# Kernel tuning notes

Hardware: AMD Instinct MI355X
Metric: run time of the kernel (lower is better)

The kernel has to match this reference:

```python
import jax, jax.numpy as jnp
import numpy as np

BIG = 1e9  # finite stand-in for float('inf') border padding (grad-safe)


def setup_inputs() -> dict:
    key = jax.random.key(0)
    k1, k2 = jax.random.split(key)
    B, L1, L2, F = 32, 1024, 1024, 128
    return {
        "seq1": jax.random.normal(k1, (B, L1, F), dtype=jnp.float32),
        "seq2": jax.random.normal(k2, (B, L2, F), dtype=jnp.float32),
        "scale_weights": jnp.ones((1,), dtype=jnp.float32),  # nn.Parameter ones(num_scales)/num_scales -> softmax-normalized anyway
    }


def _dtw_similarity(seq1, seq2):
    """Vectorized (anti-diagonal wavefront) version of MultiScaleDTW._compute_dtw.

    Same recurrence: D[i,j] = ||s1[i-1]-s2[j-1]|| + min(D[i-1,j-1], D[i-1,j], D[i,j-1]),
    D[0,0]=0, first row/col = inf. Returns similarity = 1/(1 + D[L1,L2]/(L1+L2)).
    """
    B, L1, F = seq1.shape
    L2 = seq2.shape[1]
    # pairwise L2 distance matrix (B, L1, L2) via |a|^2 + |b|^2 - 2 a.b (one GEMM)
    sq1 = jnp.sum(seq1 * seq1, axis=-1)
    sq2 = jnp.sum(seq2 * seq2, axis=-1)
    dot = jnp.einsum('bif,bjf->bij', seq1, seq2)
    C = jnp.sqrt(jnp.maximum(sq1[:, :, None] + sq2[:, None, :] - 2.0 * dot, 0.0))

    i_idx = jnp.arange(L1 + 1)
    # diagonal k holds D[i, k-i] for i in [0, L1]
    d0 = jnp.full((B, L1 + 1), BIG, jnp.float32).at[:, 0].set(0.0)  # k=0: D[0,0]=0
    d1 = jnp.full((B, L1 + 1), BIG, jnp.float32)                     # k=1: borders = inf

    def shift(x):  # x[:, i] -> x[:, i-1], pad with BIG
        return jnp.concatenate([jnp.full((B, 1), BIG, x.dtype), x[:, :-1]], axis=1)

    def step(carry, k):
        prev2, prev = carry  # diagonals k-2, k-1
        j = k - i_idx
        row = jnp.clip(i_idx - 1, 0, L1 - 1)
        col = jnp.clip(j - 1, 0, L2 - 1)
        c = C[:, row, col]  # (B, L1+1) cost along the diagonal
        m = jnp.minimum(shift(prev2), jnp.minimum(shift(prev), prev))
        cur = c + m
        valid = (i_idx >= 1) & (i_idx <= L1) & (j >= 1) & (j <= L2)
        cur = jnp.where(valid[None, :], cur, BIG)
        return (prev, cur), None

    (_, last), _ = jax.lax.scan(step, (d0, d1), jnp.arange(2, L1 + L2 + 1))
    dtw_dist = last[:, L1] / (L1 + L2)  # D[L1, L2] / (L1 + L2)
    return 1.0 / (1.0 + dtw_dist)


def reference(seq1, seq2, scale_weights):
    # num_scales = 1: softmax over single scale weight -> 1.0; only scale-0 DTW runs
    w = jax.nn.softmax(scale_weights, axis=0)
    sim = _dtw_similarity(seq1, seq2)
    return w[0] * sim  # combined_similarity, shape (B,)
```

## Files before the change

kernel.cpp:

```cpp
#include <hip/hip_runtime.h>
#include <hip/hip_bf16.h>

#define BIGV 1.0e9f

static constexpr int B_ = 32;
static constexpr int L_ = 1024;
static constexpr int F_ = 128;
static constexpr int S_ = 2;
static constexpr int UDIM_ = 1296;
static constexpr int LAG_ = 256;
static constexpr int NSEGG_ = 22;
static constexpr size_t STREAM_US = (size_t)B_ * 2 * UDIM_ * 512;

typedef __attribute__((ext_vector_type(8))) short short8;
typedef __attribute__((ext_vector_type(4))) float f32x4;

__device__ __forceinline__ unsigned pack2(float x, float y) {
  unsigned r;
  asm("v_cvt_pk_bf16_f32 %0, %1, %2" : "=v"(r) : "v"(x), "v"(y));
  return r;
}

__device__ __forceinline__ float shfl_up1_dpp(float x) {
  int xi = __float_as_int(x);
  int r = __builtin_amdgcn_update_dpp(xi, xi, 0x138, 0xF, 0xF, false);
  return __int_as_float(r);
}

__device__ __forceinline__ float min3f(float a, float b, float c) {
  float r;
  asm("v_min3_f32 %0, %1, %2, %3" : "=v"(r) : "v"(a), "v"(b), "v"(c));
  return r;
}

__global__ void norm_kernel(const float* __restrict__ s1, const float* __restrict__ s2,
                            float* __restrict__ nrm) {
  int gt   = blockIdx.x * blockDim.x + threadIdx.x;
  int wid  = gt >> 6;
  int lane = gt & 63;
  const float* src = (wid < B_ * L_) ? (s1 + (size_t)wid * F_)
                                     : (s2 + (size_t)(wid - B_ * L_) * F_);
  float2 v = ((const float2*)src)[lane];
  float s = v.x * v.x + v.y * v.y;
#pragma unroll
  for (int o = 32; o > 0; o >>= 1) s += __shfl_xor(s, o, 64);
  if (lane == 0) nrm[wid] = s;
}

__global__ __launch_bounds__(256) void cost_kernel(const float* __restrict__ s1,
                                                   const float* __restrict__ s2,
                                                   ushort* __restrict__ stream,
                                                   const float* __restrict__ nrm) {
  __shared__ __align__(16) ushort sbuf[2 * 128 * 136];
  __shared__ float q1[128], q2[128];
  short (*aL)[136] = (short(*)[136])sbuf;
  short (*bL)[136] = (short(*)[136])(sbuf + 128 * 136);
  ushort (*stage)[136] = (ushort(*)[136])sbuf;

  const int tid = threadIdx.x;
  const int b   = blockIdx.y;
  const int tc  = blockIdx.x & 7;
  const int tr  = blockIdx.x >> 3;

  const float* Ap = s1 + (size_t)b * L_ * F_ + (size_t)tr * 128 * F_;
  const float* Bp = s2 + (size_t)b * L_ * F_ + (size_t)tc * 128 * F_;

#pragma unroll 4
  for (int it = 0; it < 16; ++it) {
    int idx = it * 1024 + tid * 4;
    int r = idx >> 7, cc = idx & 127;
    float4 va = *(const float4*)(Ap + idx);
    float4 vb = *(const float4*)(Bp + idx);
    *(uint2*)&aL[r][cc] = make_uint2(pack2(va.x, va.y), pack2(va.z, va.w));
    *(uint2*)&bL[r][cc] = make_uint2(pack2(vb.x, vb.y), pack2(vb.z, vb.w));
  }
  if (tid < 128) q1[tid] = nrm[(size_t)b * L_ + tr * 128 + tid];
  else           q2[tid - 128] = nrm[(size_t)B_ * L_ + (size_t)b * L_ + tc * 128 + (tid - 128)];
  __syncthreads();

  const int wave = tid >> 6, lane = tid & 63, quad = lane >> 4, l16 = lane & 15;
  const int m0 = (wave >> 1) * 64, n0 = (wave & 1) * 64;

  f32x4 acc[4][4] = {};
#pragma unroll
  for (int kc = 0; kc < 4; ++kc) {
    short8 af[4], bf[4];
#pragma unroll
    for (int mi = 0; mi < 4; ++mi)
      af[mi] = *(const short8*)&aL[m0 + mi * 16 + l16][kc * 32 + quad * 8];
#pragma unroll
    for (int nj = 0; nj < 4; ++nj)
      bf[nj] = *(const short8*)&bL[n0 + nj * 16 + l16][kc * 32 + quad * 8];
#pragma unroll
    for (int mi = 0; mi < 4; ++mi)
#pragma unroll
      for (int nj = 0; nj < 4; ++nj)
        acc[mi][nj] = __builtin_amdgcn_mfma_f32_16x16x32_bf16(af[mi], bf[nj], acc[mi][nj], 0, 0, 0);
  }

  __syncthreads();

#pragma unroll
  for (int mi = 0; mi < 4; ++mi) {
    int lr = m0 + mi * 16 + quad * 4;
    int du = 2 * (lr >> 3);
    float a0 = q1[lr + 0], a1 = q1[lr + 1], a2 = q1[lr + 2], a3 = q1[lr + 3];
#pragma unroll
    for (int nj = 0; nj < 4; ++nj) {
      int lc = n0 + nj * 16 + l16;
      float qc = q2[lc];
      float vx = sqrtf(fmaxf(a0 + qc - 2.0f * acc[mi][nj][0], 0.0f));
      float vy = sqrtf(fmaxf(a1 + qc - 2.0f * acc[mi][nj][1], 0.0f));
      float vz = sqrtf(fmaxf(a2 + qc - 2.0f * acc[mi][nj][2], 0.0f));
      float vw = sqrtf(fmaxf(a3 + qc - 2.0f * acc[mi][nj][3], 0.0f));
      *(uint2*)&stage[lc + du][lr] = make_uint2(pack2(vx, vy), pack2(vz, vw));
    }
  }
  __syncthreads();

  const int w      = tr >> 2;
  const int rlbase = (tr & 3) * 128;
  const int ubase  = tc * 128 + 32 * (tr & 3);
  ushort* Sb = stream + ((size_t)(b * 2 + w) * UDIM_ + ubase) * 512 + rlbase;
#pragma unroll
  for (int it = 0; it < 10; ++it) {
    int t = it * 256 + tid;
    if (t < 158 * 16) {
      int u = t >> 4, g = t & 15;
      if ((unsigned)(u - 2 * g) < 128u)
        *(uint4*)(Sb + (size_t)u * 512 + g * 8) = *(const uint4*)&stage[u][g * 8];
    }
  }
}

#define UNPACK_CV(cw, cv)                         \
  cv[0] = __uint_as_float((cw).x << 16);          \
  cv[1] = __uint_as_float((cw).x & 0xFFFF0000u);  \
  cv[2] = __uint_as_float((cw).y << 16);          \
  cv[3] = __uint_as_float((cw).y & 0xFFFF0000u);  \
  cv[4] = __uint_as_float((cw).z << 16);          \
  cv[5] = __uint_as_float((cw).z & 0xFFFF0000u);  \
  cv[6] = __uint_as_float((cw).w << 16);          \
  cv[7] = __uint_as_float((cw).w & 0xFFFF0000u);

#define CHAIN_BODY(head)                                            \
  {                                                                 \
    float cur = (head);                                             \
    float nl[8];                                                    \
    nl[0] = cur;                                                    \
    _Pragma("unroll") for (int r = 1; r < 8; ++r) {                 \
      cur = cv[r] + min3f(left[r - 1], left[r], cur);               \
      nl[r] = cur;                                                  \
    }                                                               \
    _Pragma("unroll") for (int r = 0; r < 8; ++r) left[r] = nl[r];  \
    bot = nl[7];                                                    \
  }

__global__ __launch_bounds__(128, 1) void dtw_kernel(const ushort* __restrict__ stream,
                                                     float* __restrict__ out) {
  __shared__ float hand[1040];

  const int b    = blockIdx.x;
  const int tid  = threadIdx.x;
  const int wave = tid >> 6;
  const int lane = tid & 63;
  const bool l0 = (lane == 0);

  const ushort* src = stream + (size_t)(b * 2 + wave) * UDIM_ * 512 + lane * 8;

  float left[8];
#pragma unroll
  for (int r = 0; r < 8; ++r) left[r] = BIGV;
  float bot = BIGV;
  float sh[4] = {BIGV, BIGV, BIGV, BIGV};
  float hPrev = BIGV, result = 0.0f;
  float hRing[4];
  float hb[16];
  uint4 pre[16];

#pragma unroll
  for (int i = 0; i < 16; ++i) pre[i] = *(const uint4*)(src + (size_t)i * 512);

  for (int n = 0; n < NSEGG_; ++n) {
    __syncthreads();
    const int phaseS = 64 * n - (wave ? LAG_ : 0);

#pragma unroll 1
    for (int m = 0; m < 4; ++m) {
      const int sBase = phaseS + 16 * m;
      if ((unsigned)sBase >= 1152u) continue;

      const bool fast = (sBase >= 128) & (sBase <= 1008);

      if (wave == 0) {
        if (fast) {
#pragma unroll
          for (int k = 0; k < 16; ++k) {
            float shN = shfl_up1_dpp(bot);
            uint4 cw = pre[k];
            pre[k] = *(const uint4*)(src + (size_t)(sBase + k + 16) * 512);
            float cv[8];
            UNPACK_CV(cw, cv)
            float dgT = sh[(k + 2) & 3];
            float upT = sh[(k + 3) & 3];
            CHAIN_BODY(cv[0] + min3f(dgT, upT, left[0]))
            sh[k & 3] = l0 ? BIGV : shN;
            hb[k] = bot;
          }
          if (lane == 63) {
            float4* hp = (float4*)&hand[sBase - 126];
            hp[0] = make_float4(hb[0], hb[1], hb[2], hb[3]);
            hp[1] = make_float4(hb[4], hb[5], hb[6], hb[7]);
            hp[2] = make_float4(hb[8], hb[9], hb[10], hb[11]);
            hp[3] = make_float4(hb[12], hb[13], hb[14], hb[15]);
          }
        } else {
#pragma unroll
          for (int k = 0; k < 16; ++k) {
            const int s = sBase + k;
            const int col = s - S_ * lane;
            float shN = shfl_up1_dpp(bot);
            uint4 cw = pre[k];
            pre[k] = *(const uint4*)(src + (size_t)(sBase + k + 16) * 512);
            float cv[8];
            UNPACK_CV(cw, cv)
            float dgT = sh[(k + 2) & 3];
            if (l0 && s == 0) dgT = 0.0f;
            float upT = sh[(k + 3) & 3];
            bool act = ((unsigned)col < 1024u);
            float c0 = act ? cv[0] : BIGV;
            CHAIN_BODY(c0 + min3f(dgT, upT, left[0]))
            sh[k & 3] = l0 ? BIGV : shN;
            int j = s - 126;
            if (lane == 63 && (unsigned)j < 1024u) hand[j] = bot;
          }
        }
      } else {
        if (fast) {
#pragma unroll
          for (int i = 0; i < 4; ++i) hRing[i] = hand[sBase + i];
#pragma unroll
          for (int k = 0; k < 16; ++k) {
            float shN = shfl_up1_dpp(bot);
            float hCur = hRing[k & 3];
            uint4 cw = pre[k];
            pre[k] = *(const uint4*)(src + (size_t)(sBase + k + 16) * 512);
            hRing[k & 3] = hand[sBase + k + 4];
            float cv[8];
            UNPACK_CV(cw, cv)
            float dgT = l0 ? hPrev : sh[(k + 2) & 3];
            float upT = l0 ? hCur : sh[(k + 3) & 3];
            CHAIN_BODY(cv[0] + min3f(dgT, upT, left[0]))
            sh[k & 3] = shN;
            hPrev = hCur;
          }
        } else {
#pragma unroll
          for (int i = 0; i < 4; ++i) hRing[i] = hand[(sBase + i) & 1023];
#pragma unroll
          for (int k = 0; k < 16; ++k) {
            const int s = sBase + k;
            const int col = s - S_ * lane;
            float shN = shfl_up1_dpp(bot);
            float hCur = hRing[k & 3];
            uint4 cw = pre[k];
            pre[k] = *(const uint4*)(src + (size_t)(sBase + k + 16) * 512);
            hRing[k & 3] = hand[(s + 4) & 1023];
            float cv[8];
            UNPACK_CV(cw, cv)
            float dgT = l0 ? ((s == 0) ? BIGV : hPrev) : sh[(k + 2) & 3];
            float upT = l0 ? hCur : sh[(k + 3) & 3];
            bool act = ((unsigned)col < 1024u);
            float c0 = act ? cv[0] : BIGV;
            CHAIN_BODY(c0 + min3f(dgT, upT, left[0]))
            sh[k & 3] = shN;
            hPrev = hCur;
            if (s == 1149) result = bot;
          }
        }
      }
    }
  }
  if (wave == 1 && lane == 63) out[b] = 1.0f / (1.0f + result * (1.0f / 2048.0f));
}

extern "C" void kernel_launch(void* const* d_in, const int* in_sizes, int n_in,
                              void* d_out, int out_size, void* d_ws, size_t ws_size,
                              hipStream_t stream_) {
  const float* s1 = (const float*)d_in[0];
  const float* s2 = (const float*)d_in[1];
  float* out = (float*)d_out;
  ushort* cws = (ushort*)d_ws;
  float* nrm = (float*)(cws + STREAM_US);

  norm_kernel<<<dim3((2 * B_ * L_) / 4), 256, 0, stream_>>>(s1, s2, nrm);
  cost_kernel<<<dim3(64, B_), 256, 0, stream_>>>(s1, s2, cws, nrm);
  dtw_kernel<<<dim3(B_), 128, 0, stream_>>>(cws, out);
}
```

Before: 236.8 us.

## Process two DTW columns per lane per step with paired cost stream layout

Each lane now handles two adjacent columns per wavefront step instead of one. This halves the number of serial steps, from a skew of 2 per lane to 1 per lane, and shortens the inter-wave lag. The cost kernel pairs adjacent columns with a DPP swap and writes interleaved bf16 pairs into a re-laid-out stream. The aim is to cut the wavefront's pipeline fill overhead and the per-step shuffle and sync cost, at the price of more registers for the doubled prefetch buffers and more complex indexing.

```diff
diff --git a/kernel.cpp b/kernel.cpp
--- a/kernel.cpp
+++ b/kernel.cpp
@@ -6,11 +6,10 @@
 static constexpr int B_ = 32;
 static constexpr int L_ = 1024;
 static constexpr int F_ = 128;
-static constexpr int S_ = 2;
-static constexpr int UDIM_ = 1296;
-static constexpr int LAG_ = 256;
-static constexpr int NSEGG_ = 22;
-static constexpr size_t STREAM_US = (size_t)B_ * 2 * UDIM_ * 512;
+static constexpr int UD2_ = 592;
+static constexpr int LAGP_ = 96;
+static constexpr int NSEGP_ = 42;
+static constexpr size_t STREAM_US = (size_t)B_ * 2 * UD2_ * 1024;
 
 typedef __attribute__((ext_vector_type(8))) short short8;
 typedef __attribute__((ext_vector_type(4))) float f32x4;
@@ -24,6 +23,12 @@
 __device__ __forceinline__ float shfl_up1_dpp(float x) {
   int xi = __float_as_int(x);
   int r = __builtin_amdgcn_update_dpp(xi, xi, 0x138, 0xF, 0xF, false);
+  return __int_as_float(r);
+}
+
+__device__ __forceinline__ float dpp_odd(float x) {
+  int xi = __float_as_int(x);
+  int r = __builtin_amdgcn_update_dpp(xi, xi, 0xF5, 0xF, 0xF, false);
   return __int_as_float(r);
 }
 
@@ -55,7 +60,7 @@
   __shared__ float q1[128], q2[128];
   short (*aL)[136] = (short(*)[136])sbuf;
   short (*bL)[136] = (short(*)[136])(sbuf + 128 * 136);
-  ushort (*stage)[136] = (ushort(*)[136])sbuf;
+  ushort (*stage)[256] = (ushort(*)[256])sbuf;
 
   const int tid = threadIdx.x;
   const int b   = blockIdx.y;
@@ -102,58 +107,66 @@
 
 #pragma unroll
   for (int mi = 0; mi < 4; ++mi) {
-    int lr = m0 + mi * 16 + quad * 4;
-    int du = 2 * (lr >> 3);
-    float a0 = q1[lr + 0], a1 = q1[lr + 1], a2 = q1[lr + 2], a3 = q1[lr + 3];
+    int lr0 = m0 + mi * 16 + quad * 4;
+    float a0 = q1[lr0 + 0], a1 = q1[lr0 + 1], a2 = q1[lr0 + 2], a3 = q1[lr0 + 3];
 #pragma unroll
     for (int nj = 0; nj < 4; ++nj) {
       int lc = n0 + nj * 16 + l16;
       float qc = q2[lc];
-      float vx = sqrtf(fmaxf(a0 + qc - 2.0f * acc[mi][nj][0], 0.0f));
-      float vy = sqrtf(fmaxf(a1 + qc - 2.0f * acc[mi][nj][1], 0.0f));
-      float vz = sqrtf(fmaxf(a2 + qc - 2.0f * acc[mi][nj][2], 0.0f));
-      float vw = sqrtf(fmaxf(a3 + qc - 2.0f * acc[mi][nj][3], 0.0f));
-      *(uint2*)&stage[lc + du][lr] = make_uint2(pack2(vx, vy), pack2(vz, vw));
+      float v0 = sqrtf(fmaxf(a0 + qc - 2.0f * acc[mi][nj][0], 0.0f));
+      float v1 = sqrtf(fmaxf(a1 + qc - 2.0f * acc[mi][nj][1], 0.0f));
+      float v2 = sqrtf(fmaxf(a2 + qc - 2.0f * acc[mi][nj][2], 0.0f));
+      float v3 = sqrtf(fmaxf(a3 + qc - 2.0f * acc[mi][nj][3], 0.0f));
+      float o0 = dpp_odd(v0), o1 = dpp_odd(v1), o2 = dpp_odd(v2), o3 = dpp_odd(v3);
+      if ((l16 & 1) == 0) {
+        int u = (lr0 >> 3) + (lc >> 1);
+        uint4 wd = make_uint4(pack2(v0, o0), pack2(v1, o1), pack2(v2, o2), pack2(v3, o3));
+        *(uint4*)&stage[u][lr0 * 2] = wd;
+      }
     }
   }
   __syncthreads();
 
-  const int w      = tr >> 2;
-  const int rlbase = (tr & 3) * 128;
-  const int ubase  = tc * 128 + 32 * (tr & 3);
-  ushort* Sb = stream + ((size_t)(b * 2 + w) * UDIM_ + ubase) * 512 + rlbase;
+  const int w        = tr >> 2;
+  const int slotbase = 256 * (tr & 3);
+  const int ubase    = tc * 64 + 16 * (tr & 3);
+  ushort* Sb = stream + ((size_t)(b * 2 + w) * UD2_ + ubase) * 1024 + slotbase;
 #pragma unroll
   for (int it = 0; it < 10; ++it) {
     int t = it * 256 + tid;
-    if (t < 158 * 16) {
-      int u = t >> 4, g = t & 15;
-      if ((unsigned)(u - 2 * g) < 128u)
-        *(uint4*)(Sb + (size_t)u * 512 + g * 8) = *(const uint4*)&stage[u][g * 8];
+    if (t < 80 * 32) {
+      int u = t >> 5, h = t & 31, g = h >> 1;
+      if ((unsigned)(u - g) < 64u)
+        *(uint4*)(Sb + (size_t)u * 1024 + g * 16 + (h & 1) * 8) =
+            *(const uint4*)&stage[u][g * 16 + (h & 1) * 8];
     }
   }
 }
 
-#define UNPACK_CV(cw, cv)                         \
-  cv[0] = __uint_as_float((cw).x << 16);          \
-  cv[1] = __uint_as_float((cw).x & 0xFFFF0000u);  \
-  cv[2] = __uint_as_float((cw).y << 16);          \
-  cv[3] = __uint_as_float((cw).y & 0xFFFF0000u);  \
-  cv[4] = __uint_as_float((cw).z << 16);          \
-  cv[5] = __uint_as_float((cw).z & 0xFFFF0000u);  \
-  cv[6] = __uint_as_float((cw).w << 16);          \
-  cv[7] = __uint_as_float((cw).w & 0xFFFF0000u);
-
-#define CHAIN_BODY(head)                                            \
+#define PAIR_STEP(C0HEAD, C1HEAD)                                   \
   {                                                                 \
-    float cur = (head);                                             \
-    float nl[8];                                                    \
-    nl[0] = cur;                                                    \
+    unsigned wds[8] = {cwA.x, cwA.y, cwA.z, cwA.w,                  \
+                       cwB.x, cwB.y, cwB.z, cwB.w};                 \
+    float cv0[8], cv1[8];                                           \
+    _Pragma("unroll") for (int r = 0; r < 8; ++r) {                 \
+      cv0[r] = __uint_as_float(wds[r] << 16);                       \
+      cv1[r] = __uint_as_float(wds[r] & 0xFFFF0000u);               \
+    }                                                               \
+    float nlA[8], nlB[8];                                           \
+    float curA = (C0HEAD) + min3f(dg0, up0, left[0]);               \
+    nlA[0] = curA;                                                  \
     _Pragma("unroll") for (int r = 1; r < 8; ++r) {                 \
-      cur = cv[r] + min3f(left[r - 1], left[r], cur);               \
-      nl[r] = cur;                                                  \
+      curA = cv0[r] + min3f(left[r - 1], left[r], curA);            \
+      nlA[r] = curA;                                                \
     }                                                               \
-    _Pragma("unroll") for (int r = 0; r < 8; ++r) left[r] = nl[r];  \
-    bot = nl[7];                                                    \
+    float curB = (C1HEAD) + min3f(up0, up1, nlA[0]);                \
+    nlB[0] = curB;                                                  \
+    _Pragma("unroll") for (int r = 1; r < 8; ++r) {                 \
+      curB = cv1[r] + min3f(nlA[r - 1], nlA[r], curB);              \
+      nlB[r] = curB;                                                \
+    }                                                               \
+    _Pragma("unroll") for (int r = 0; r < 8; ++r) left[r] = nlB[r]; \
+    bot0 = nlA[7]; bot1 = nlB[7];                                   \
   }
 
 __global__ __launch_bounds__(128, 1) void dtw_kernel(const ushort* __restrict__ stream,
@@ -166,117 +179,118 @@
   const int lane = tid & 63;
   const bool l0 = (lane == 0);
 
-  const ushort* src = stream + (size_t)(b * 2 + wave) * UDIM_ * 512 + lane * 8;
+  const ushort* src = stream + (size_t)(b * 2 + wave) * UD2_ * 1024 + lane * 16;
 
   float left[8];
 #pragma unroll
   for (int r = 0; r < 8; ++r) left[r] = BIGV;
-  float bot = BIGV;
-  float sh[4] = {BIGV, BIGV, BIGV, BIGV};
-  float hPrev = BIGV, result = 0.0f;
-  float hRing[4];
-  float hb[16];
-  uint4 pre[16];
-
-#pragma unroll
-  for (int i = 0; i < 16; ++i) pre[i] = *(const uint4*)(src + (size_t)i * 512);
-
-  for (int n = 0; n < NSEGG_; ++n) {
+  float bot0 = BIGV, bot1 = BIGV;
+  float shAprev = BIGV, hPv = BIGV, result = 0.0f;
+  float2 hR[4];
+  float hb0[16], hb1[16];
+  uint4 pre0[16], pre1[16];
+
+#pragma unroll
+  for (int i = 0; i < 16; ++i) {
+    pre0[i] = *(const uint4*)(src + (size_t)i * 1024);
+    pre1[i] = *(const uint4*)(src + (size_t)i * 1024 + 8);
+  }
+
+  for (int n = 0; n < NSEGP_; ++n) {
     __syncthreads();
-    const int phaseS = 64 * n - (wave ? LAG_ : 0);
-
-#pragma unroll 1
-    for (int m = 0; m < 4; ++m) {
-      const int sBase = phaseS + 16 * m;
-      if ((unsigned)sBase >= 1152u) continue;
-
-      const bool fast = (sBase >= 128) & (sBase <= 1008);
-
-      if (wave == 0) {
-        if (fast) {
-#pragma unroll
-          for (int k = 0; k < 16; ++k) {
-            float shN = shfl_up1_dpp(bot);
-            uint4 cw = pre[k];
-            pre[k] = *(const uint4*)(src + (size_t)(sBase + k + 16) * 512);
-            float cv[8];
-            UNPACK_CV(cw, cv)
-            float dgT = sh[(k + 2) & 3];
-            float upT = sh[(k + 3) & 3];
-            CHAIN_BODY(cv[0] + min3f(dgT, upT, left[0]))
-            sh[k & 3] = l0 ? BIGV : shN;
-            hb[k] = bot;
+    const int tBase = 16 * n - (wave ? LAGP_ : 0);
+    if ((unsigned)tBase >= 576u) continue;
+
+    const bool fast = (tBase >= 64) & (tBase <= 496);
+
+    if (wave == 0) {
+      if (fast) {
+#pragma unroll
+        for (int k = 0; k < 16; ++k) {
+          float shA = shfl_up1_dpp(bot1);
+          float shB = shfl_up1_dpp(bot0);
+          uint4 cwA = pre0[k], cwB = pre1[k];
+          const ushort* p = src + (size_t)(tBase + k + 16) * 1024;
+          pre0[k] = *(const uint4*)p;
+          pre1[k] = *(const uint4*)(p + 8);
+          float dg0 = l0 ? BIGV : shAprev;
+          float up0 = l0 ? BIGV : shB;
+          float up1 = l0 ? BIGV : shA;
+          PAIR_STEP(cv0[0], cv1[0])
+          shAprev = shA;
+          hb0[k] = bot0; hb1[k] = bot1;
+        }
+        if (lane == 63) {
+          float2* hp = (float2*)&hand[2 * tBase - 126];
+#pragma unroll
+          for (int q = 0; q < 16; ++q) hp[q] = make_float2(hb0[q], hb1[q]);
+        }
+      } else {
+#pragma unroll
+        for (int k = 0; k < 16; ++k) {
+          const int t = tBase + k;
+          float shA = shfl_up1_dpp(bot1);
+          float shB = shfl_up1_dpp(bot0);
+          uint4 cwA = pre0[k], cwB = pre1[k];
+          const ushort* p = src + (size_t)(tBase + k + 16) * 1024;
+          pre0[k] = *(const uint4*)p;
+          pre1[k] = *(const uint4*)(p + 8);
+          float dg0 = l0 ? ((t == 0) ? 0.0f : BIGV) : shAprev;
+          float up0 = l0 ? BIGV : shB;
+          float up1 = l0 ? BIGV : shA;
+          bool act = ((unsigned)(t - lane) < 512u);
+          PAIR_STEP(act ? cv0[0] : BIGV, act ? cv1[0] : BIGV)
+          shAprev = shA;
+          int j = 2 * t - 126;
+          if (lane == 63 && (unsigned)j < 1024u) {
+            hand[j] = bot0; hand[j + 1] = bot1;
           }
-          if (lane == 63) {
-            float4* hp = (float4*)&hand[sBase - 126];
-            hp[0] = make_float4(hb[0], hb[1], hb[2], hb[3]);
-            hp[1] = make_float4(hb[4], hb[5], hb[6], hb[7]);
-            hp[2] = make_float4(hb[8], hb[9], hb[10], hb[11]);
-            hp[3] = make_float4(hb[12], hb[13], hb[14], hb[15]);
-          }
-        } else {
-#pragma unroll
-          for (int k = 0; k < 16; ++k) {
-            const int s = sBase + k;
-            const int col = s - S_ * lane;
-            float shN = shfl_up1_dpp(bot);
-            uint4 cw = pre[k];
-            pre[k] = *(const uint4*)(src + (size_t)(sBase + k + 16) * 512);
-            float cv[8];
-            UNPACK_CV(cw, cv)
-            float dgT = sh[(k + 2) & 3];
-            if (l0 && s == 0) dgT = 0.0f;
-            float upT = sh[(k + 3) & 3];
-            bool act = ((unsigned)col < 1024u);
-            float c0 = act ? cv[0] : BIGV;
-            CHAIN_BODY(c0 + min3f(dgT, upT, left[0]))
-            sh[k & 3] = l0 ? BIGV : shN;
-            int j = s - 126;
-            if (lane == 63 && (unsigned)j < 1024u) hand[j] = bot;
-          }
+        }
+      }
+    } else {
+      if (fast) {
+#pragma unroll
+        for (int i = 0; i < 4; ++i) hR[i] = *(const float2*)&hand[2 * (tBase + i)];
+#pragma unroll
+        for (int k = 0; k < 16; ++k) {
+          float shA = shfl_up1_dpp(bot1);
+          float shB = shfl_up1_dpp(bot0);
+          float2 hCur = hR[k & 3];
+          uint4 cwA = pre0[k], cwB = pre1[k];
+          const ushort* p = src + (size_t)(tBase + k + 16) * 1024;
+          pre0[k] = *(const uint4*)p;
+          pre1[k] = *(const uint4*)(p + 8);
+          hR[k & 3] = *(const float2*)&hand[2 * (tBase + k + 4)];
+          float dg0 = l0 ? hPv : shAprev;
+          float up0 = l0 ? hCur.x : shB;
+          float up1 = l0 ? hCur.y : shA;
+          PAIR_STEP(cv0[0], cv1[0])
+          shAprev = shA;
+          hPv = hCur.y;
         }
       } else {
-        if (fast) {
-#pragma unroll
-          for (int i = 0; i < 4; ++i) hRing[i] = hand[sBase + i];
-#pragma unroll
-          for (int k = 0; k < 16; ++k) {
-            float shN = shfl_up1_dpp(bot);
-            float hCur = hRing[k & 3];
-            uint4 cw = pre[k];
-            pre[k] = *(const uint4*)(src + (size_t)(sBase + k + 16) * 512);
-            hRing[k & 3] = hand[sBase + k + 4];
-            float cv[8];
-            UNPACK_CV(cw, cv)
-            float dgT = l0 ? hPrev : sh[(k + 2) & 3];
-            float upT = l0 ? hCur : sh[(k + 3) & 3];
-            CHAIN_BODY(cv[0] + min3f(dgT, upT, left[0]))
-            sh[k & 3] = shN;
-            hPrev = hCur;
-          }
-        } else {
-#pragma unroll
-          for (int i = 0; i < 4; ++i) hRing[i] = hand[(sBase + i) & 1023];
-#pragma unroll
-          for (int k = 0; k < 16; ++k) {
-            const int s = sBase + k;
-            const int col = s - S_ * lane;
-            float shN = shfl_up1_dpp(bot);
-            float hCur = hRing[k & 3];
-            uint4 cw = pre[k];
-            pre[k] = *(const uint4*)(src + (size_t)(sBase + k + 16) * 512);
-            hRing[k & 3] = hand[(s + 4) & 1023];
-            float cv[8];
-            UNPACK_CV(cw, cv)
-            float dgT = l0 ? ((s == 0) ? BIGV : hPrev) : sh[(k + 2) & 3];
-            float upT = l0 ? hCur : sh[(k + 3) & 3];
-            bool act = ((unsigned)col < 1024u);
-            float c0 = act ? cv[0] : BIGV;
-            CHAIN_BODY(c0 + min3f(dgT, upT, left[0]))
-            sh[k & 3] = shN;
-            hPrev = hCur;
-            if (s == 1149) result = bot;
-          }
+#pragma unroll
+        for (int i = 0; i < 4; ++i)
+          hR[i] = *(const float2*)&hand[(2 * (tBase + i)) & 1023];
+#pragma unroll
+        for (int k = 0; k < 16; ++k) {
+          const int t = tBase + k;
+          float shA = shfl_up1_dpp(bot1);
+          float shB = shfl_up1_dpp(bot0);
+          float2 hCur = hR[k & 3];
+          uint4 cwA = pre0[k], cwB = pre1[k];
+          const ushort* p = src + (size_t)(tBase + k + 16) * 1024;
+          pre0[k] = *(const uint4*)p;
+          pre1[k] = *(const uint4*)(p + 8);
+          hR[k & 3] = *(const float2*)&hand[(2 * (t + 4)) & 1023];
+          float dg0 = l0 ? hPv : shAprev;
+          float up0 = l0 ? hCur.x : shB;
+          float up1 = l0 ? hCur.y : shA;
+          bool act = ((unsigned)(t - lane) < 512u);
+          PAIR_STEP(act ? cv0[0] : BIGV, act ? cv1[0] : BIGV)
+          shAprev = shA;
+          hPv = hCur.y;
+          if (t == 574) result = bot1;
         }
       }
     }
```

After: 223.4 us. 1.06x faster.
